# Kernel tuning notes

Hardware: AMD Instinct MI355X
Metric: run time of the kernel (lower is better)

The kernel has to match this reference:

```python
import jax, jax.numpy as jnp
import numpy as np

N_NODES = 100000
N_EDGES = 800000
DIM = 128
BN_EPS = 1e-5


def setup_inputs() -> dict:
    key = jax.random.key(0)
    k1, k2, k3 = jax.random.split(key, 3)
    x = jax.random.normal(k1, (N_NODES, DIM), dtype=jnp.float32)
    edge_index = jax.random.randint(k2, (2, N_EDGES), 0, N_NODES, dtype=jnp.int64)
    # xavier-uniform-like init for the linear weight [out, in]
    limit = float(np.sqrt(6.0 / (DIM + DIM)))
    W = jax.random.uniform(k3, (DIM, DIM), dtype=jnp.float32, minval=-limit, maxval=limit)
    bias = jnp.zeros((DIM,), dtype=jnp.float32)
    bn_gamma = jnp.ones((DIM,), dtype=jnp.float32)
    bn_beta = jnp.zeros((DIM,), dtype=jnp.float32)
    return {"x": x, "edge_index": edge_index, "W": W, "bias": bias,
            "bn_gamma": bn_gamma, "bn_beta": bn_beta, "bit_sum": 0}


def reference(x, edge_index, W, bias, bn_gamma, bn_beta, bit_sum):
    n = x.shape[0]
    # Linear (no bias), is_q=False path; q_xw treated as identity.
    h = x @ W.T                                   # [N, D]
    row, col = edge_index[0], edge_index[1]
    # symmetric degree normalization: deg computed over destination (col)
    deg = jax.ops.segment_sum(jnp.ones_like(col, dtype=h.dtype), col, num_segments=n)
    deg_inv_sqrt = jnp.where(deg > 0, jax.lax.rsqrt(jnp.maximum(deg, 1.0)), 0.0)
    norm = deg_inv_sqrt[row] * deg_inv_sqrt[col]  # [E]
    # message: norm * x_j (x_j = h[row]), aggregate (add) at col
    msg = norm[:, None] * h[row]                  # [E, D]
    out = jax.ops.segment_sum(msg, col, num_segments=n)  # [N, D]
    out = out + bias
    # BatchNorm1d (training mode: batch stats, biased variance)
    mean = jnp.mean(out, axis=0)
    var = jnp.var(out, axis=0)
    out = (out - mean) * jax.lax.rsqrt(var + BN_EPS) * bn_gamma + bn_beta
    # activation
    out = jax.nn.relu(out)
    # residual (in_dim == out_dim); dropout p=0 -> identity
    out = out + x
    return (out, 0)
```

## Files before the change

kernel.cpp:

```cpp
#include <hip/hip_runtime.h>
#include <cstddef>

#define NN 100000
#define DD 128
#define ND (NN * DD)
#define BN_EPS 1e-5f
#define LDA 136
#define NREP 16
#define NBKT 98
#define EPB 4096

typedef __bf16 bf16_t;
typedef bf16_t bf16x8 __attribute__((ext_vector_type(8)));
typedef float f32x4 __attribute__((ext_vector_type(4)));
typedef unsigned int uint;
typedef unsigned short ushort;


__device__ __forceinline__ ushort f2b(float f) {
    uint u = __builtin_bit_cast(uint, f);
    u += 0x7FFFu + ((u >> 16) & 1u);
    return (ushort)(u >> 16);
}
__device__ __forceinline__ float b2f(uint s) {
    return __builtin_bit_cast(float, s << 16);
}

__device__ __forceinline__ int detect_i64(const int* __restrict__ ei) {
    __shared__ int sflag;
    int t = threadIdx.x;
    if (t < 64) {
        int hi = ei[2 * t + 1];
        unsigned long long b = __ballot(hi == 0);
        if (t == 0) sflag = (b == ~0ull) ? 1 : 0;
    }
    __syncthreads();
    return sflag;
}

__global__ __launch_bounds__(256) void k_prep(const int* __restrict__ ei,
                                              int* __restrict__ bktot, int E, int nbh,
                                              const float* __restrict__ x,
                                              uint* __restrict__ xb,
                                              const float* __restrict__ W,
                                              uint* __restrict__ wb) {
    if ((int)blockIdx.x < nbh) {
        int f = detect_i64(ei);
        __shared__ int hist[NBKT];
        int t = threadIdx.x;
        if (t < NBKT) hist[t] = 0;
        __syncthreads();
        int base = blockIdx.x * EPB;
        int count = min(EPB, E - base);
        for (int i = t; i < count; i += 256) {
            int e = base + i;
            int c = f ? ei[2 * (E + e)] : ei[E + e];
            atomicAdd(&hist[c >> 10], 1);
        }
        __syncthreads();
        if (t < NBKT && hist[t] > 0) atomicAdd(&bktot[t], hist[t]);
        return;
    }
    int i = (blockIdx.x - nbh) * 256 + threadIdx.x;
    const float* src;
    uint* dst;
    int j;
    if (i < ND / 8) { src = x; dst = xb; j = i; }
    else { j = i - ND / 8; if (j >= (DD * DD) / 8) return; src = W; dst = wb; }
    const float4* s4 = (const float4*)src;
    float4 a = s4[2 * j], b = s4[2 * j + 1];
    uint4 o;
    o.x = (uint)f2b(a.x) | ((uint)f2b(a.y) << 16);
    o.y = (uint)f2b(a.z) | ((uint)f2b(a.w) << 16);
    o.z = (uint)f2b(b.x) | ((uint)f2b(b.y) << 16);
    o.w = (uint)f2b(b.z) | ((uint)f2b(b.w) << 16);
    ((uint4*)dst)[j] = o;
}

__global__ __launch_bounds__(256) void k_bin(const int* __restrict__ ei,
                                             const int* __restrict__ bktot,
                                             int* __restrict__ bcur,
                                             uint2* __restrict__ pairs, int E) {
    int f = detect_i64(ei);
    __shared__ int bb[NBKT], hist[NBKT], scur[NBKT];
    int t = threadIdx.x;
    if (t < NBKT) { bb[t] = bktot[t]; hist[t] = 0; }
    __syncthreads();
    if (t == 0) {
        int run = 0;
        for (int i = 0; i < NBKT; ++i) { int v = bb[i]; bb[i] = run; run += v; }
    }
    int base = blockIdx.x * EPB;
    int count = min(EPB, E - base);
    int rr[16], cc[16];
#pragma unroll
    for (int k = 0; k < 16; ++k) {
        int i = t + k * 256;
        if (i < count) {
            int e = base + i;
            int r, c;
            if (f) { r = ei[2 * e]; c = ei[2 * (E + e)]; }
            else   { r = ei[e];     c = ei[E + e]; }
            rr[k] = r; cc[k] = c;
            atomicAdd(&hist[c >> 10], 1);
        }
    }
    __syncthreads();
    if (t < NBKT) scur[t] = bb[t] + atomicAdd(&bcur[t], hist[t]);
    __syncthreads();
#pragma unroll
    for (int k = 0; k < 16; ++k) {
        int i = t + k * 256;
        if (i < count) {
            int b = cc[k] >> 10;
            int pos = atomicAdd(&scur[b], 1);
            pairs[pos] = (uint2){(uint)rr[k], (uint)cc[k]};
        }
    }
}

__global__ __launch_bounds__(256) void k_cnt(const uint2* __restrict__ pairs,
                                             const int* __restrict__ bktot,
                                             int* __restrict__ ptr0,
                                             int* __restrict__ cnt,
                                             float* __restrict__ dinv,
                                             int* __restrict__ srow) {
    __shared__ int hist[1024];
    __shared__ int scur[1024];
    __shared__ int ls[256];
    __shared__ int bb[NBKT];
    __shared__ int se0, se1;
    int b = blockIdx.x;
    int t = threadIdx.x;
    if (t < NBKT) bb[t] = bktot[t];
#pragma unroll
    for (int i = 0; i < 4; ++i) hist[t + i * 256] = 0;
    __syncthreads();
    if (t == 0) {
        int run = 0;
        for (int i = 0; i < b; ++i) run += bb[i];
        se0 = run; se1 = run + bb[b];
    }
    __syncthreads();
    int e0 = se0, e1 = se1;
    int nodebase = b << 10;
    for (int i = e0 + t; i < e1; i += 256)
        atomicAdd(&hist[(int)pairs[i].y - nodebase], 1);
    __syncthreads();
    int c4[4];
    int lsum = 0;
#pragma unroll
    for (int i = 0; i < 4; ++i) { c4[i] = hist[t * 4 + i]; lsum += c4[i]; }
    ls[t] = lsum;
    __syncthreads();
    for (int o = 1; o < 256; o <<= 1) {
        int v = (t >= o) ? ls[t - o] : 0;
        __syncthreads();
        ls[t] += v;
        __syncthreads();
    }
    int run = ls[t] - lsum + e0;
#pragma unroll
    for (int i = 0; i < 4; ++i) {
        int idx = nodebase + t * 4 + i;
        if (idx < NN) {
            ptr0[idx] = run;
            cnt[idx] = c4[i];
            dinv[idx] = c4[i] > 0 ? rsqrtf((float)c4[i]) : 0.f;
        }
        scur[t * 4 + i] = run;
        run += c4[i];
    }
    __syncthreads();
    for (int i = e0 + t; i < e1; i += 256) {
        uint2 p = pairs[i];
        int pos = atomicAdd(&scur[(int)p.y - nodebase], 1);
        srow[pos] = (int)p.x;
    }
}

__global__ __launch_bounds__(512, 8) void k_gg(const uint* __restrict__ xb,
                                               const int* __restrict__ srow,
                                               const int* __restrict__ ptr0,
                                               const int* __restrict__ cnt,
                                               const float* __restrict__ dinv,
                                               const ushort* __restrict__ wb,
                                               ushort* __restrict__ hb,
                                               float* __restrict__ csr,
                                               float* __restrict__ cqr) {
    __shared__ char smem[64 * LDA * 2];
    ushort* sAp = (ushort*)smem;
    int t = threadIdx.x;
    int wave = t >> 6, lane = t & 63;
    uint rowbase = (uint)blockIdx.x * 64;

    int mn = (int)rowbase + wave * 8 + (lane & 7);
    int sv = 0, kv = 0;
    float dv = 0.f;
    if (lane < 8 && mn < NN) { sv = ptr0[mn]; kv = cnt[mn]; dv = dinv[mn]; }

    for (int i = 0; i < 8; i += 2) {
        int sa0 = __shfl(sv, i),     kA = __shfl(kv, i);
        int sb0 = __shfl(sv, i + 1), kB = __shfl(kv, i + 1);
        float dA = __shfl(dv, i), dB = __shfl(dv, i + 1);
        float axA = 0.f, ayA = 0.f, axB = 0.f, ayB = 0.f;
        int kmax = max(kA, kB);
        for (int base = 0; base < kmax; base += 64) {
            int mA = kA - base; mA = mA > 64 ? 64 : mA;
            int mB = kB - base; mB = mB > 64 ? 64 : mB;
            int rjA = 0, rjB = 0;
            if (lane < mA) rjA = srow[sa0 + base + lane];
            if (lane < mB) rjB = srow[sb0 + base + lane];
            int mm = max(mA, mB);
            for (int j = 0; j < mm; j += 4) {
                int ra0 = __shfl(rjA, j),     rb0 = __shfl(rjB, j);
                int ra1 = __shfl(rjA, j + 1), rb1 = __shfl(rjB, j + 1);
                int ra2 = __shfl(rjA, j + 2), rb2 = __shfl(rjB, j + 2);
                int ra3 = __shfl(rjA, j + 3), rb3 = __shfl(rjB, j + 3);
                uint va0 = xb[((uint)ra0 << 6) + (uint)lane];
                uint vb0 = xb[((uint)rb0 << 6) + (uint)lane];
                uint va1 = xb[((uint)ra1 << 6) + (uint)lane];
                uint vb1 = xb[((uint)rb1 << 6) + (uint)lane];
                uint va2 = xb[((uint)ra2 << 6) + (uint)lane];
                uint vb2 = xb[((uint)rb2 << 6) + (uint)lane];
                uint va3 = xb[((uint)ra3 << 6) + (uint)lane];
                uint vb3 = xb[((uint)rb3 << 6) + (uint)lane];
                float wa0 = dinv[ra0], wbb0 = dinv[rb0];
                float wa1 = dinv[ra1], wbb1 = dinv[rb1];
                float wa2 = dinv[ra2], wbb2 = dinv[rb2];
                float wa3 = dinv[ra3], wbb3 = dinv[rb3];
                wa0 = (j     < mA) ? wa0 : 0.f;  wbb0 = (j     < mB) ? wbb0 : 0.f;
                wa1 = (j + 1 < mA) ? wa1 : 0.f;  wbb1 = (j + 1 < mB) ? wbb1 : 0.f;
                wa2 = (j + 2 < mA) ? wa2 : 0.f;  wbb2 = (j + 2 < mB) ? wbb2 : 0.f;
                wa3 = (j + 3 < mA) ? wa3 : 0.f;  wbb3 = (j + 3 < mB) ? wbb3 : 0.f;
                axA = fmaf(wa0, b2f(va0 & 0xFFFFu), axA); ayA = fmaf(wa0, b2f(va0 >> 16), ayA);
                axA = fmaf(wa1, b2f(va1 & 0xFFFFu), axA); ayA = fmaf(wa1, b2f(va1 >> 16), ayA);
                axA = fmaf(wa2, b2f(va2 & 0xFFFFu), axA); ayA = fmaf(wa2, b2f(va2 >> 16), ayA);
                axA = fmaf(wa3, b2f(va3 & 0xFFFFu), axA); ayA = fmaf(wa3, b2f(va3 >> 16), ayA);
                axB = fmaf(wbb0, b2f(vb0 & 0xFFFFu), axB); ayB = fmaf(wbb0, b2f(vb0 >> 16), ayB);
                axB = fmaf(wbb1, b2f(vb1 & 0xFFFFu), axB); ayB = fmaf(wbb1, b2f(vb1 >> 16), ayB);
                axB = fmaf(wbb2, b2f(vb2 & 0xFFFFu), axB); ayB = fmaf(wbb2, b2f(vb2 >> 16), ayB);
                axB = fmaf(wbb3, b2f(vb3 & 0xFFFFu), axB); ayB = fmaf(wbb3, b2f(vb3 >> 16), ayB);
            }
        }
        *(uint*)(sAp + (wave * 8 + i) * LDA + lane * 2) =
            (uint)f2b(dA * axA) | ((uint)f2b(dA * ayA) << 16);
        *(uint*)(sAp + (wave * 8 + i + 1) * LDA + lane * 2) =
            (uint)f2b(dB * axB) | ((uint)f2b(dB * ayB) << 16);
    }
    __syncthreads();

    int rg = wave & 3, chh = wave >> 2;
    int quad = lane >> 4, l16 = lane & 15;
    bf16x8 Af[4];
#pragma unroll
    for (int ks = 0; ks < 4; ++ks)
        Af[ks] = __builtin_bit_cast(
            bf16x8, *(const uint4*)(sAp + (rg * 16 + l16) * LDA + ks * 32 + quad * 8));
    __syncthreads();
    float (*cp)[64] = (float (*)[64])smem;
    float (*cq)[64] = (float (*)[64])(smem + 8 * 64 * 4);

#pragma unroll
    for (int c = 0; c < 4; ++c) {
        int ctg = chh * 4 + c;
        bf16x8 Bf[4];
#pragma unroll
        for (int ks = 0; ks < 4; ++ks)
            Bf[ks] = __builtin_bit_cast(
                bf16x8,
                *(const uint4*)(wb + (uint)(ctg * 16 + l16) * 128 + ks * 32 + quad * 8));
        f32x4 acc = (f32x4){0.f, 0.f, 0.f, 0.f};
#pragma unroll
        for (int ks = 0; ks < 4; ++ks)
            acc = __builtin_amdgcn_mfma_f32_16x16x32_bf16(Af[ks], Bf[ks], acc, 0, 0, 0);
        float ss = 0.f, qq = 0.f;
#pragma unroll
        for (int r = 0; r < 4; ++r) {
            float v = acc[r];
            ss += v; qq += v * v;
            uint row = rowbase + rg * 16 + quad * 4 + r;
            if (row < NN) hb[row * 128u + (uint)(ctg * 16 + l16)] = f2b(v);
        }
        ss += __shfl_xor(ss, 16); ss += __shfl_xor(ss, 32);
        qq += __shfl_xor(qq, 16); qq += __shfl_xor(qq, 32);
        if (quad == 0) { cp[wave][c * 16 + l16] = ss; cq[wave][c * 16 + l16] = qq; }
    }
    __syncthreads();
    if (t < 128) {
        int w0 = (t >> 6) * 4, lc = t & 63;
        float s = cp[w0][lc] + cp[w0 + 1][lc] + cp[w0 + 2][lc] + cp[w0 + 3][lc];
        float q = cq[w0][lc] + cq[w0 + 1][lc] + cq[w0 + 2][lc] + cq[w0 + 3][lc];
        int rep = (blockIdx.x & (NREP - 1)) * 128 + t;
        atomicAdd(&csr[rep], s);
        atomicAdd(&cqr[rep], q);
    }
}

__global__ __launch_bounds__(256) void k_final(const uint* __restrict__ hb,
                                               const uint* __restrict__ xb,
                                               const float* __restrict__ gamma,
                                               const float* __restrict__ beta,
                                               const float* __restrict__ csr,
                                               const float* __restrict__ cqr,
                                               float* __restrict__ out, int out_size) {
    __shared__ float sa[128], sb[128];
    int t = threadIdx.x;
    const float invN = 1.0f / NN;
    if (t < 128) {
        float s = 0.f;
        for (int i = 0; i < NREP; ++i) s += csr[i * 128 + t];
        sa[t] = s * invN;
    } else {
        int c = t - 128;
        float s = 0.f;
        for (int i = 0; i < NREP; ++i) s += cqr[i * 128 + c];
        sb[c] = s * invN;
    }
    __syncthreads();
    if (t < 128) {
        float m = sa[t];
        float var = sb[t] - m * m;
        float inv = rsqrtf(var + BN_EPS);
        float A = inv * gamma[t];
        float B = beta[t] - m * A;
        sa[t] = A; sb[t] = B;
    }
    __syncthreads();

    int c0 = (t & 7) * 16;
    int u8 = blockIdx.x * 512 + t * 2;
    uint4 hv0 = ((const uint4*)hb)[u8], hv1 = ((const uint4*)hb)[u8 + 1];
    uint4 xv0 = ((const uint4*)xb)[u8], xv1 = ((const uint4*)xb)[u8 + 1];
    uint hu[8] = {hv0.x, hv0.y, hv0.z, hv0.w, hv1.x, hv1.y, hv1.z, hv1.w};
    uint xu[8] = {xv0.x, xv0.y, xv0.z, xv0.w, xv1.x, xv1.y, xv1.z, xv1.w};
    float res[16];
#pragma unroll
    for (int p = 0; p < 8; ++p) {
        int c = c0 + p * 2;
        float h0 = b2f(hu[p] & 0xFFFFu), h1 = b2f(hu[p] >> 16);
        float x0 = b2f(xu[p] & 0xFFFFu), x1 = b2f(xu[p] >> 16);
        res[2 * p]     = fmaxf(fmaf(h0, sa[c],     sb[c]),     0.f) + x0;
        res[2 * p + 1] = fmaxf(fmaf(h1, sa[c + 1], sb[c + 1]), 0.f) + x1;
    }
    float4* o4 = (float4*)out;
    int ob = blockIdx.x * 1024 + t * 4;
#pragma unroll
    for (int q = 0; q < 4; ++q)
        o4[ob + q] = (float4){res[4 * q], res[4 * q + 1], res[4 * q + 2], res[4 * q + 3]};
    if (blockIdx.x == 0 && t == 0 && out_size > ND) out[ND] = 0.0f;
}

extern "C" void kernel_launch(void* const* d_in, const int* in_sizes, int n_in,
                              void* d_out, int out_size, void* d_ws, size_t ws_size,
                              hipStream_t stream) {
    const float* x     = (const float*)d_in[0];
    const int*   ei    = (const int*)d_in[1];
    const float* W     = (const float*)d_in[2];
    const float* gamma = (const float*)d_in[4];
    const float* beta  = (const float*)d_in[5];
    float* ws = (float*)d_ws;
    float* out = (float*)d_out;

    uint*   hb       = (uint*)ws;
    uint*   xb       = hb + ND / 2;
    float*  csr      = (float*)(xb + ND / 2);
    float*  cqr      = csr + NREP * 128;
    int*    bktot    = (int*)(cqr + NREP * 128);
    int*    bcur     = bktot + 128;
    int*    cnt      = bcur + 128;
    int*    ptr0     = cnt + NN;
    float*  dinv     = (float*)(ptr0 + NN);
    int*    srow     = (int*)(dinv + NN);

    int E = in_sizes[1] / 2;
    uint* wb = (uint*)(srow + E);

    uint2* pairs = (uint2*)hb;

    int nbc = (ND / 8 + (DD * DD) / 8 + 255) / 256;
    int nbin = (E + EPB - 1) / EPB;

    hipMemsetAsync(csr, 0, (size_t)(2 * NREP * 128 + 256) * 4, stream);
    k_prep<<<nbin + nbc, 256, 0, stream>>>(ei, bktot, E, nbin, x, xb, W, wb);
    k_bin<<<nbin, 256, 0, stream>>>(ei, bktot, bcur, pairs, E);
    k_cnt<<<NBKT, 256, 0, stream>>>(pairs, bktot, ptr0, cnt, dinv, srow);
    k_gg<<<(NN + 63) / 64, 512, 0, stream>>>(xb, srow, ptr0, cnt, dinv,
                                             (const ushort*)wb, (ushort*)hb, csr, cqr);
    k_final<<<ND / 4096, 256, 0, stream>>>(hb, xb, gamma, beta, csr, cqr,
                                           out, out_size);
}
```

Measured before the change: 227.7 us.

## Fuse gather-GEMM and BatchNorm epilogue into one cooperative persistent kernel

Replaces the separate gather/GEMM kernel and the final BatchNorm kernel with a single cooperative kernel. Each block processes up to four 64-row tiles, keeps the bf16 results in registers, performs a grid-wide sync once the column statistics are accumulated, and then applies normalization, ReLU and the residual add directly. This removes the bf16 h write and re-read through global memory and one kernel launch. In exchange it adds register pressure, lowers the launch bound to 4 blocks, introduces a grid barrier, and uses a scattered output store pattern instead of float4 stores.

```diff
diff --git a/kernel.cpp b/kernel.cpp
--- a/kernel.cpp
+++ b/kernel.cpp
@@ -1,5 +1,8 @@
 #include <hip/hip_runtime.h>
+#include <hip/hip_cooperative_groups.h>
 #include <cstddef>
+
+namespace cg = cooperative_groups;
 
 #define NN 100000
 #define DD 128
@@ -9,6 +12,8 @@
 #define NREP 16
 #define NBKT 98
 #define EPB 4096
+#define NT ((NN + 63) / 64)
+#define TMAX 4
 
 typedef __bf16 bf16_t;
 typedef bf16_t bf16x8 __attribute__((ext_vector_type(8)));
@@ -179,20 +184,20 @@
     }
 }
 
-__global__ __launch_bounds__(512, 8) void k_gg(const uint* __restrict__ xb,
-                                               const int* __restrict__ srow,
-                                               const int* __restrict__ ptr0,
-                                               const int* __restrict__ cnt,
-                                               const float* __restrict__ dinv,
-                                               const ushort* __restrict__ wb,
-                                               ushort* __restrict__ hb,
-                                               float* __restrict__ csr,
-                                               float* __restrict__ cqr) {
-    __shared__ char smem[64 * LDA * 2];
+__device__ __forceinline__ void tile_compute(int tile, int wave, int lane,
+                                             const uint* __restrict__ xb,
+                                             const int* __restrict__ srow,
+                                             const int* __restrict__ ptr0,
+                                             const int* __restrict__ cnt,
+                                             const float* __restrict__ dinv,
+                                             const ushort* __restrict__ wb,
+                                             float* __restrict__ csr,
+                                             float* __restrict__ cqr,
+                                             char* smem, uint* hp,
+                                             ushort* __restrict__ hb) {
     ushort* sAp = (ushort*)smem;
-    int t = threadIdx.x;
-    int wave = t >> 6, lane = t & 63;
-    uint rowbase = (uint)blockIdx.x * 64;
+    int t = wave * 64 + lane;
+    uint rowbase = (uint)tile * 64;
 
     int mn = (int)rowbase + wave * 8 + (lane & 7);
     int sv = 0, kv = 0;
@@ -276,11 +281,16 @@
             acc = __builtin_amdgcn_mfma_f32_16x16x32_bf16(Af[ks], Bf[ks], acc, 0, 0, 0);
         float ss = 0.f, qq = 0.f;
 #pragma unroll
-        for (int r = 0; r < 4; ++r) {
-            float v = acc[r];
-            ss += v; qq += v * v;
-            uint row = rowbase + rg * 16 + quad * 4 + r;
-            if (row < NN) hb[row * 128u + (uint)(ctg * 16 + l16)] = f2b(v);
+        for (int r = 0; r < 4; ++r) { float v = acc[r]; ss += v; qq += v * v; }
+        if (hp) {
+            hp[c * 2]     = (uint)f2b(acc[0]) | ((uint)f2b(acc[1]) << 16);
+            hp[c * 2 + 1] = (uint)f2b(acc[2]) | ((uint)f2b(acc[3]) << 16);
+        } else {
+#pragma unroll
+            for (int r = 0; r < 4; ++r) {
+                uint row = rowbase + rg * 16 + quad * 4 + r;
+                if (row < NN) hb[row * 128u + (uint)(ctg * 16 + l16)] = f2b(acc[r]);
+            }
         }
         ss += __shfl_xor(ss, 16); ss += __shfl_xor(ss, 32);
         qq += __shfl_xor(qq, 16); qq += __shfl_xor(qq, 32);
@@ -291,10 +301,109 @@
         int w0 = (t >> 6) * 4, lc = t & 63;
         float s = cp[w0][lc] + cp[w0 + 1][lc] + cp[w0 + 2][lc] + cp[w0 + 3][lc];
         float q = cq[w0][lc] + cq[w0 + 1][lc] + cq[w0 + 2][lc] + cq[w0 + 3][lc];
-        int rep = (blockIdx.x & (NREP - 1)) * 128 + t;
+        int rep = (tile & (NREP - 1)) * 128 + t;
         atomicAdd(&csr[rep], s);
         atomicAdd(&cqr[rep], q);
     }
+    __syncthreads();
+}
+
+__device__ __forceinline__ void tile_epilogue(int tile, int wave, int lane,
+                                              const ushort* __restrict__ xbs,
+                                              const float* sa, const float* sb,
+                                              float* __restrict__ out,
+                                              const uint hp[8]) {
+    uint rowbase = (uint)tile * 64;
+    int rg = wave & 3, chh = wave >> 2;
+    int quad = lane >> 4, l16 = lane & 15;
+#pragma unroll
+    for (int c = 0; c < 4; ++c) {
+        int col = chh * 64 + c * 16 + l16;
+        float A = sa[col], B = sb[col];
+#pragma unroll
+        for (int r = 0; r < 4; ++r) {
+            uint row = rowbase + rg * 16 + quad * 4 + r;
+            if (row < NN) {
+                float h = b2f((hp[c * 2 + (r >> 1)] >> ((r & 1) * 16)) & 0xFFFFu);
+                float xv = b2f((uint)xbs[row * 128u + (uint)col]);
+                out[row * 128u + (uint)col] = fmaxf(fmaf(h, A, B), 0.f) + xv;
+            }
+        }
+    }
+}
+
+__global__ __launch_bounds__(512, 4) void k_ggf(const uint* __restrict__ xb,
+                                                const int* __restrict__ srow,
+                                                const int* __restrict__ ptr0,
+                                                const int* __restrict__ cnt,
+                                                const float* __restrict__ dinv,
+                                                const ushort* __restrict__ wb,
+                                                float* __restrict__ csr,
+                                                float* __restrict__ cqr,
+                                                const float* __restrict__ gamma,
+                                                const float* __restrict__ beta,
+                                                float* __restrict__ out, int out_size) {
+    __shared__ char smem[64 * LDA * 2];
+    int t = threadIdx.x;
+    int wave = t >> 6, lane = t & 63;
+    int bid = blockIdx.x, g = gridDim.x;
+
+    uint hp[TMAX][8];
+#pragma unroll
+    for (int i = 0; i < TMAX; ++i) {
+        int tile = bid + i * g;
+        if (tile < NT)
+            tile_compute(tile, wave, lane, xb, srow, ptr0, cnt, dinv, wb, csr, cqr,
+                         smem, hp[i], nullptr);
+    }
+
+    __threadfence();
+    cg::this_grid().sync();
+
+    float* sa = (float*)smem;
+    float* sb = sa + 128;
+    const float invN = 1.0f / NN;
+    if (t < 128) {
+        float s = 0.f;
+        for (int i = 0; i < NREP; ++i)
+            s += __hip_atomic_load(&csr[i * 128 + t], __ATOMIC_RELAXED,
+                                   __HIP_MEMORY_SCOPE_AGENT);
+        float q = 0.f;
+        for (int i = 0; i < NREP; ++i)
+            q += __hip_atomic_load(&cqr[i * 128 + t], __ATOMIC_RELAXED,
+                                   __HIP_MEMORY_SCOPE_AGENT);
+        float m = s * invN;
+        float var = q * invN - m * m;
+        float inv = rsqrtf(var + BN_EPS);
+        float A = inv * gamma[t];
+        sa[t] = A;
+        sb[t] = beta[t] - m * A;
+    }
+    __syncthreads();
+
+    const ushort* xbs = (const ushort*)xb;
+#pragma unroll
+    for (int i = 0; i < TMAX; ++i) {
+        int tile = bid + i * g;
+        if (tile < NT)
+            tile_epilogue(tile, wave, lane, xbs, sa, sb, out, hp[i]);
+    }
+    if (bid == 0 && t == 0 && out_size > ND) out[ND] = 0.0f;
+}
+
+__global__ __launch_bounds__(512, 4) void k_gg(const uint* __restrict__ xb,
+                                               const int* __restrict__ srow,
+                                               const int* __restrict__ ptr0,
+                                               const int* __restrict__ cnt,
+                                               const float* __restrict__ dinv,
+                                               const ushort* __restrict__ wb,
+                                               ushort* __restrict__ hb,
+                                               float* __restrict__ csr,
+                                               float* __restrict__ cqr) {
+    __shared__ char smem[64 * LDA * 2];
+    int t = threadIdx.x;
+    tile_compute(blockIdx.x, t >> 6, t & 63, xb, srow, ptr0, cnt, dinv, wb, csr, cqr,
+                 smem, nullptr, hb);
 }
 
 __global__ __launch_bounds__(256) void k_final(const uint* __restrict__ hb,
@@ -362,8 +471,8 @@
     float* ws = (float*)d_ws;
     float* out = (float*)d_out;
 
-    uint*   hb       = (uint*)ws;
-    uint*   xb       = hb + ND / 2;
+    uint*   region0  = (uint*)ws;
+    uint*   xb       = region0 + ND / 2;
     float*  csr      = (float*)(xb + ND / 2);
     float*  cqr      = csr + NREP * 128;
     int*    bktot    = (int*)(cqr + NREP * 128);
@@ -375,8 +484,7 @@
 
     int E = in_sizes[1] / 2;
     uint* wb = (uint*)(srow + E);
-
-    uint2* pairs = (uint2*)hb;
+    uint2* pairs = (uint2*)region0;
 
     int nbc = (ND / 8 + (DD * DD) / 8 + 255) / 256;
     int nbin = (E + EPB - 1) / EPB;
@@ -385,8 +493,44 @@
     k_prep<<<nbin + nbc, 256, 0, stream>>>(ei, bktot, E, nbin, x, xb, W, wb);
     k_bin<<<nbin, 256, 0, stream>>>(ei, bktot, bcur, pairs, E);
     k_cnt<<<NBKT, 256, 0, stream>>>(pairs, bktot, ptr0, cnt, dinv, srow);
-    k_gg<<<(NN + 63) / 64, 512, 0, stream>>>(xb, srow, ptr0, cnt, dinv,
-                                             (const ushort*)wb, (ushort*)hb, csr, cqr);
-    k_final<<<ND / 4096, 256, 0, stream>>>(hb, xb, gamma, beta, csr, cqr,
-                                           out, out_size);
-}
+
+    static int coopGrid = -2;
+    if (coopGrid == -2) {
+        int nb = 0;
+        if (hipOccupancyMaxActiveBlocksPerMultiprocessor(&nb, (const void*)k_ggf,
+                                                         512, 0) != hipSuccess)
+            nb = 0;
+        long g = (long)nb * 256;
+        if (g > 1024) g = 1024;
+        coopGrid = (g > 0 && g * TMAX >= NT) ? (int)g : 0;
+    }
+
+    bool done = false;
+    if (coopGrid > 0) {
+        const uint*   a_xb   = xb;
+        const int*    a_srow = srow;
+        const int*    a_ptr0 = ptr0;
+        const int*    a_cnt  = cnt;
+        const float*  a_dinv = dinv;
+        const ushort* a_wb   = (const ushort*)wb;
+        float*        a_csr  = csr;
+        float*        a_cqr  = cqr;
+        const float*  a_g    = gamma;
+        const float*  a_b    = beta;
+        float*        a_out  = out;
+        int           a_os   = out_size;
+        void* args[] = {(void*)&a_xb, (void*)&a_srow, (void*)&a_ptr0, (void*)&a_cnt,
+                        (void*)&a_dinv, (void*)&a_wb, (void*)&a_csr, (void*)&a_cqr,
+                        (void*)&a_g, (void*)&a_b, (void*)&a_out, (void*)&a_os};
+        hipError_t err = hipLaunchCooperativeKernel((void*)k_ggf, dim3(coopGrid),
+                                                    dim3(512), args, 0, stream);
+        if (err == hipSuccess) done = true;
+        else coopGrid = 0;
+    }
+    if (!done) {
+        k_gg<<<NT, 512, 0, stream>>>(xb, srow, ptr0, cnt, dinv, (const ushort*)wb,
+                                     (ushort*)region0, csr, cqr);
+        k_final<<<ND / 4096, 256, 0, stream>>>(region0, xb, gamma, beta, csr, cqr,
+                                               out, out_size);
+    }
+}
```

After: 227.9 us. About the same (+0.1%).

## Gather neighbor rows with 16-byte loads, four nodes per wave

Applied to the files above, without the earlier changes.

The gather-aggregate loop now splits each wave into four 16-lane groups. Each group handles one destination node and loads a full 256-byte bf16 row as uint4 per lane, instead of one uint per lane across 64 lanes for two nodes at a time. This cuts the number of load instructions, and the shuffle and dinv overhead per edge, at the cost of more accumulator registers (eight per lane). The launch-bounds occupancy hint drops from 8 to 4. Shared memory for the partial-statistics buffers is now separate instead of aliased, which removes one barrier. The groups in a wave are padded to the largest degree among their four nodes.

```diff
diff --git a/kernel.cpp b/kernel.cpp
--- a/kernel.cpp
+++ b/kernel.cpp
@@ -9,6 +9,7 @@
 #define NREP 16
 #define NBKT 98
 #define EPB 4096
+#define NT ((NN + 63) / 64)
 
 typedef __bf16 bf16_t;
 typedef bf16_t bf16x8 __attribute__((ext_vector_type(8)));
@@ -24,6 +25,12 @@
 }
 __device__ __forceinline__ float b2f(uint s) {
     return __builtin_bit_cast(float, s << 16);
+}
+__device__ __forceinline__ float blo(uint u) {
+    return __builtin_bit_cast(float, u << 16);
+}
+__device__ __forceinline__ float bhi(uint u) {
+    return __builtin_bit_cast(float, u & 0xFFFF0000u);
 }
 
 __device__ __forceinline__ int detect_i64(const int* __restrict__ ei) {
@@ -179,7 +186,7 @@
     }
 }
 
-__global__ __launch_bounds__(512, 8) void k_gg(const uint* __restrict__ xb,
+__global__ __launch_bounds__(512, 4) void k_gg(const uint* __restrict__ xb,
                                                const int* __restrict__ srow,
                                                const int* __restrict__ ptr0,
                                                const int* __restrict__ cnt,
@@ -188,78 +195,65 @@
                                                ushort* __restrict__ hb,
                                                float* __restrict__ csr,
                                                float* __restrict__ cqr) {
-    __shared__ char smem[64 * LDA * 2];
-    ushort* sAp = (ushort*)smem;
+    __shared__ ushort sA[64 * LDA];
+    __shared__ float cp[8][64], cq[8][64];
     int t = threadIdx.x;
     int wave = t >> 6, lane = t & 63;
+    int quad = lane >> 4, l16 = lane & 15;
     uint rowbase = (uint)blockIdx.x * 64;
+    const uint4* xb4 = (const uint4*)xb;
 
     int mn = (int)rowbase + wave * 8 + (lane & 7);
     int sv = 0, kv = 0;
     float dv = 0.f;
     if (lane < 8 && mn < NN) { sv = ptr0[mn]; kv = cnt[mn]; dv = dinv[mn]; }
 
-    for (int i = 0; i < 8; i += 2) {
-        int sa0 = __shfl(sv, i),     kA = __shfl(kv, i);
-        int sb0 = __shfl(sv, i + 1), kB = __shfl(kv, i + 1);
-        float dA = __shfl(dv, i), dB = __shfl(dv, i + 1);
-        float axA = 0.f, ayA = 0.f, axB = 0.f, ayB = 0.f;
-        int kmax = max(kA, kB);
-        for (int base = 0; base < kmax; base += 64) {
-            int mA = kA - base; mA = mA > 64 ? 64 : mA;
-            int mB = kB - base; mB = mB > 64 ? 64 : mB;
-            int rjA = 0, rjB = 0;
-            if (lane < mA) rjA = srow[sa0 + base + lane];
-            if (lane < mB) rjB = srow[sb0 + base + lane];
-            int mm = max(mA, mB);
-            for (int j = 0; j < mm; j += 4) {
-                int ra0 = __shfl(rjA, j),     rb0 = __shfl(rjB, j);
-                int ra1 = __shfl(rjA, j + 1), rb1 = __shfl(rjB, j + 1);
-                int ra2 = __shfl(rjA, j + 2), rb2 = __shfl(rjB, j + 2);
-                int ra3 = __shfl(rjA, j + 3), rb3 = __shfl(rjB, j + 3);
-                uint va0 = xb[((uint)ra0 << 6) + (uint)lane];
-                uint vb0 = xb[((uint)rb0 << 6) + (uint)lane];
-                uint va1 = xb[((uint)ra1 << 6) + (uint)lane];
-                uint vb1 = xb[((uint)rb1 << 6) + (uint)lane];
-                uint va2 = xb[((uint)ra2 << 6) + (uint)lane];
-                uint vb2 = xb[((uint)rb2 << 6) + (uint)lane];
-                uint va3 = xb[((uint)ra3 << 6) + (uint)lane];
-                uint vb3 = xb[((uint)rb3 << 6) + (uint)lane];
-                float wa0 = dinv[ra0], wbb0 = dinv[rb0];
-                float wa1 = dinv[ra1], wbb1 = dinv[rb1];
-                float wa2 = dinv[ra2], wbb2 = dinv[rb2];
-                float wa3 = dinv[ra3], wbb3 = dinv[rb3];
-                wa0 = (j     < mA) ? wa0 : 0.f;  wbb0 = (j     < mB) ? wbb0 : 0.f;
-                wa1 = (j + 1 < mA) ? wa1 : 0.f;  wbb1 = (j + 1 < mB) ? wbb1 : 0.f;
-                wa2 = (j + 2 < mA) ? wa2 : 0.f;  wbb2 = (j + 2 < mB) ? wbb2 : 0.f;
-                wa3 = (j + 3 < mA) ? wa3 : 0.f;  wbb3 = (j + 3 < mB) ? wbb3 : 0.f;
-                axA = fmaf(wa0, b2f(va0 & 0xFFFFu), axA); ayA = fmaf(wa0, b2f(va0 >> 16), ayA);
-                axA = fmaf(wa1, b2f(va1 & 0xFFFFu), axA); ayA = fmaf(wa1, b2f(va1 >> 16), ayA);
-                axA = fmaf(wa2, b2f(va2 & 0xFFFFu), axA); ayA = fmaf(wa2, b2f(va2 >> 16), ayA);
-                axA = fmaf(wa3, b2f(va3 & 0xFFFFu), axA); ayA = fmaf(wa3, b2f(va3 >> 16), ayA);
-                axB = fmaf(wbb0, b2f(vb0 & 0xFFFFu), axB); ayB = fmaf(wbb0, b2f(vb0 >> 16), ayB);
-                axB = fmaf(wbb1, b2f(vb1 & 0xFFFFu), axB); ayB = fmaf(wbb1, b2f(vb1 >> 16), ayB);
-                axB = fmaf(wbb2, b2f(vb2 & 0xFFFFu), axB); ayB = fmaf(wbb2, b2f(vb2 >> 16), ayB);
-                axB = fmaf(wbb3, b2f(vb3 & 0xFFFFu), axB); ayB = fmaf(wbb3, b2f(vb3 >> 16), ayB);
+    for (int bt = 0; bt < 2; ++bt) {
+        int ni = bt * 4 + quad;
+        int s_here = __shfl(sv, ni);
+        int k_here = __shfl(kv, ni);
+        float d_here = __shfl(dv, ni);
+        int km = max(k_here, __shfl_xor(k_here, 16));
+        km = max(km, __shfl_xor(km, 32));
+
+        float ax0 = 0.f, ax1 = 0.f, ax2 = 0.f, ax3 = 0.f;
+        float ax4 = 0.f, ax5 = 0.f, ax6 = 0.f, ax7 = 0.f;
+
+        for (int base = 0; base < km; base += 16) {
+            int rem = k_here - base;
+            int rj = 0;
+            if (l16 < rem) rj = srow[s_here + base + l16];
+            int jend = km - base; jend = jend > 16 ? 16 : jend;
+            for (int j = 0; j < jend; j += 4) {
+#pragma unroll
+                for (int u = 0; u < 4; ++u) {
+                    int jj = j + u;
+                    int rsel = __shfl(rj, (lane & 48) + jj);
+                    float w = dinv[rsel];
+                    uint4 v = xb4[((uint)rsel << 4) + (uint)l16];
+                    w = (jj < rem) ? w : 0.f;
+                    ax0 = fmaf(w, blo(v.x), ax0); ax1 = fmaf(w, bhi(v.x), ax1);
+                    ax2 = fmaf(w, blo(v.y), ax2); ax3 = fmaf(w, bhi(v.y), ax3);
+                    ax4 = fmaf(w, blo(v.z), ax4); ax5 = fmaf(w, bhi(v.z), ax5);
+                    ax6 = fmaf(w, blo(v.w), ax6); ax7 = fmaf(w, bhi(v.w), ax7);
+                }
             }
         }
-        *(uint*)(sAp + (wave * 8 + i) * LDA + lane * 2) =
-            (uint)f2b(dA * axA) | ((uint)f2b(dA * ayA) << 16);
-        *(uint*)(sAp + (wave * 8 + i + 1) * LDA + lane * 2) =
-            (uint)f2b(dB * axB) | ((uint)f2b(dB * ayB) << 16);
+        uint4 o;
+        o.x = (uint)f2b(d_here * ax0) | ((uint)f2b(d_here * ax1) << 16);
+        o.y = (uint)f2b(d_here * ax2) | ((uint)f2b(d_here * ax3) << 16);
+        o.z = (uint)f2b(d_here * ax4) | ((uint)f2b(d_here * ax5) << 16);
+        o.w = (uint)f2b(d_here * ax6) | ((uint)f2b(d_here * ax7) << 16);
+        *(uint4*)(sA + (wave * 8 + ni) * LDA + l16 * 8) = o;
     }
     __syncthreads();
 
     int rg = wave & 3, chh = wave >> 2;
-    int quad = lane >> 4, l16 = lane & 15;
     bf16x8 Af[4];
 #pragma unroll
     for (int ks = 0; ks < 4; ++ks)
         Af[ks] = __builtin_bit_cast(
-            bf16x8, *(const uint4*)(sAp + (rg * 16 + l16) * LDA + ks * 32 + quad * 8));
-    __syncthreads();
-    float (*cp)[64] = (float (*)[64])smem;
-    float (*cq)[64] = (float (*)[64])(smem + 8 * 64 * 4);
+            bf16x8, *(const uint4*)(sA + (rg * 16 + l16) * LDA + ks * 32 + quad * 8));
 
 #pragma unroll
     for (int c = 0; c < 4; ++c) {
@@ -291,7 +285,7 @@
         int w0 = (t >> 6) * 4, lc = t & 63;
         float s = cp[w0][lc] + cp[w0 + 1][lc] + cp[w0 + 2][lc] + cp[w0 + 3][lc];
         float q = cq[w0][lc] + cq[w0 + 1][lc] + cq[w0 + 2][lc] + cq[w0 + 3][lc];
-        int rep = (blockIdx.x & (NREP - 1)) * 128 + t;
+        int rep = ((int)blockIdx.x & (NREP - 1)) * 128 + t;
         atomicAdd(&csr[rep], s);
         atomicAdd(&cqr[rep], q);
     }
@@ -338,8 +332,8 @@
 #pragma unroll
     for (int p = 0; p < 8; ++p) {
         int c = c0 + p * 2;
-        float h0 = b2f(hu[p] & 0xFFFFu), h1 = b2f(hu[p] >> 16);
-        float x0 = b2f(xu[p] & 0xFFFFu), x1 = b2f(xu[p] >> 16);
+        float h0 = blo(hu[p]), h1 = bhi(hu[p]);
+        float x0 = blo(xu[p]), x1 = bhi(xu[p]);
         res[2 * p]     = fmaxf(fmaf(h0, sa[c],     sb[c]),     0.f) + x0;
         res[2 * p + 1] = fmaxf(fmaf(h1, sa[c + 1], sb[c + 1]), 0.f) + x1;
     }
@@ -362,8 +356,8 @@
     float* ws = (float*)d_ws;
     float* out = (float*)d_out;
 
-    uint*   hb       = (uint*)ws;
-    uint*   xb       = hb + ND / 2;
+    uint*   region0  = (uint*)ws;
+    uint*   xb       = region0 + ND / 2;
     float*  csr      = (float*)(xb + ND / 2);
     float*  cqr      = csr + NREP * 128;
     int*    bktot    = (int*)(cqr + NREP * 128);
@@ -375,8 +369,7 @@
 
     int E = in_sizes[1] / 2;
     uint* wb = (uint*)(srow + E);
-
-    uint2* pairs = (uint2*)hb;
+    uint2* pairs = (uint2*)region0;
 
     int nbc = (ND / 8 + (DD * DD) / 8 + 255) / 256;
     int nbin = (E + EPB - 1) / EPB;
@@ -385,8 +378,8 @@
     k_prep<<<nbin + nbc, 256, 0, stream>>>(ei, bktot, E, nbin, x, xb, W, wb);
     k_bin<<<nbin, 256, 0, stream>>>(ei, bktot, bcur, pairs, E);
     k_cnt<<<NBKT, 256, 0, stream>>>(pairs, bktot, ptr0, cnt, dinv, srow);
-    k_gg<<<(NN + 63) / 64, 512, 0, stream>>>(xb, srow, ptr0, cnt, dinv,
-                                             (const ushort*)wb, (ushort*)hb, csr, cqr);
-    k_final<<<ND / 4096, 256, 0, stream>>>(hb, xb, gamma, beta, csr, cqr,
+    k_gg<<<NT, 512, 0, stream>>>(xb, srow, ptr0, cnt, dinv, (const ushort*)wb,
+                                 (ushort*)region0, csr, cqr);
+    k_final<<<ND / 4096, 256, 0, stream>>>(region0, xb, gamma, beta, csr, cqr,
                                            out, out_size);
 }
```

After: 224.0 us. About the same (-1.6%).
